# Performance work log

Hardware: AMD Instinct MI355X
Metric: run time of the kernel (lower is better)

## Reference

```python
import jax, jax.numpy as jnp
import numpy as np

EMBED = 1024
HEADS = 16
HEAD_DIM = EMBED // HEADS


def setup_inputs() -> dict:
    key = jax.random.key(0)
    ks = jax.random.split(key, 12)
    B, S, E = 2, 2048, EMBED
    scale = 1.0 / np.sqrt(E)
    inp = {
        "query": jax.random.normal(ks[0], (B, S, E), jnp.float32),
        "key": jax.random.normal(ks[1], (B, S, E), jnp.float32),
        "value": jax.random.normal(ks[2], (B, S, E), jnp.float32),
        "Wq": jax.random.normal(ks[3], (E, E), jnp.float32) * scale,
        "bq": jax.random.normal(ks[4], (E,), jnp.float32) * 0.01,
        "Wk": jax.random.normal(ks[5], (E, E), jnp.float32) * scale,
        "bk": jax.random.normal(ks[6], (E,), jnp.float32) * 0.01,
        "Wv": jax.random.normal(ks[7], (E, E), jnp.float32) * scale,
        "bv": jax.random.normal(ks[8], (E,), jnp.float32) * 0.01,
        "Wo": jax.random.normal(ks[9], (E, E), jnp.float32) * scale,
        "bo": jax.random.normal(ks[10], (E,), jnp.float32) * 0.01,
    }
    return inp


def reference(query, key, value, Wq, bq, Wk, bk, Wv, bv, Wo, bo):
    B, Sq, E = query.shape
    Sk = key.shape[1]
    H, D = HEADS, HEAD_DIM
    # QKV projections (torch Linear: x @ W.T + b)
    q = (query @ Wq.T + bq).reshape(B, Sq, H, D)
    k = (key @ Wk.T + bk).reshape(B, Sk, H, D)
    v = (value @ Wv.T + bv).reshape(B, Sk, H, D)
    # energy: [B, H, Sq, Sk]; note scale = 1/sqrt(embed_size), not head_dim
    energy = jnp.einsum("bqhd,bkhd->bhqk", q, k)
    scale = jnp.asarray(E, energy.dtype) ** 0.5
    attn = jax.nn.softmax(energy / scale, axis=-1)
    out = jnp.einsum("bhqk,bkhd->bqhd", attn, v).reshape(B, Sq, E)
    # fc_out (dropout is identity at eval)
    return out @ Wo.T + bo
```

## Files before the change

kernel.cpp:

```cpp
#include <hip/hip_runtime.h>
#include <hip/hip_bf16.h>

typedef __hip_bfloat16 bf16;
typedef short frag8 __attribute__((ext_vector_type(8)));
typedef _Float16 half4 __attribute__((ext_vector_type(4)));
typedef __fp16 fp16x2 __attribute__((ext_vector_type(2)));
typedef float f32x4 __attribute__((ext_vector_type(4)));

typedef __attribute__((address_space(3))) void lds_void;
typedef __attribute__((address_space(1))) const void gbl_void;

__device__ __forceinline__ void gld16(const void* g, void* l) {
  __builtin_amdgcn_global_load_lds((gbl_void*)g, (lds_void*)l, 16, 0, 0);
}

__device__ __forceinline__ unsigned short f2bf(float f) {
  union { float f; unsigned u; } x; x.f = f;
  unsigned r = x.u + 0x7FFFu + ((x.u >> 16) & 1u);
  return (unsigned short)(r >> 16);
}

#define QSCALE 0.0450842200278f
#define MFIX 4.0f

struct CvtArgs {
  const float4* src[7];
  ushort4* dst[7];
  int n4[7];
};
__global__ __launch_bounds__(256) void cvt_all(CvtArgs a) {
  const int t = blockIdx.y;
  const int i = blockIdx.x * 256 + threadIdx.x;
  if (i >= a.n4[t]) return;
  float4 v = a.src[t][i];
  ushort4 o;
  o.x = f2bf(v.x); o.y = f2bf(v.y); o.z = f2bf(v.z); o.w = f2bf(v.w);
  a.dst[t][i] = o;
}

template<int IH>
__device__ __forceinline__ void mfma16i(f32x4 (&acc)[8][4], const frag8 (&a4)[4], const frag8 (&b4)[4]) {
  __builtin_amdgcn_s_setprio(1);
  #pragma unroll
  for (int i = 0; i < 4; ++i) {
    #pragma unroll
    for (int j = 0; j < 4; ++j)
      acc[IH * 4 + i][j] = __builtin_amdgcn_mfma_f32_16x16x32_bf16(a4[i], b4[j], acc[IH * 4 + i][j], 0, 0, 0);
  }
  __builtin_amdgcn_s_setprio(0);
}

__global__ __launch_bounds__(512, 2)
void gemm_qkv256(const bf16* __restrict__ A0, const bf16* __restrict__ A1, const bf16* __restrict__ A2,
                 const bf16* __restrict__ W0, const bf16* __restrict__ W1, const bf16* __restrict__ W2,
                 const float* __restrict__ b0, const float* __restrict__ b1, const float* __restrict__ b2,
                 void* __restrict__ o0, void* __restrict__ o1, void* __restrict__ o2) {
  __shared__ __align__(16) bf16 As[2][16384];
  __shared__ __align__(16) bf16 Bs[2][16384];
  const int tid = threadIdx.x;
  const int wave = tid >> 6, lane = tid & 63, quad = lane >> 4, l16 = lane & 15;
  const int wm = wave >> 2, wn = wave & 3;
  const int bn = blockIdx.x, bm = blockIdx.y, z = blockIdx.z;

  const bf16* A = A0; const bf16* W = W0; const float* bias = b0; void* out = o0;
  if (z == 1) { A = A1; W = W1; bias = b1; out = o1; }
  else if (z == 2) { A = A2; W = W2; bias = b2; out = o2; }

  const bf16* Ab = A + (size_t)bm * 256 * 1024;
  const bf16* Wb = W + (size_t)bn * 256 * 1024;
  const int c0_ = tid & 3, r0_ = tid >> 2;
  const int gcp = ((c0_ ^ ((r0_ >> 1) & 3)) << 3);
  const int rc2 = (quad ^ ((l16 >> 1) & 3)) << 3;

  auto stage = [&](const bf16* src, int kt, int kh, bf16* dst) {
    #pragma unroll
    for (int is = 0; is < 2; ++is) {
      const int r = r0_ + is * 128;
      gld16(src + (size_t)r * 1024 + kt * 64 + kh * 32 + gcp,
            (void*)(dst + (is * 512 + tid) * 8));
    }
  };
  auto ldsA4 = [&](const bf16* ah, int ih, frag8 (&a4)[4]) {
    #pragma unroll
    for (int i = 0; i < 4; ++i)
      a4[i] = *(const frag8*)&ah[(wm * 128 + ih * 64 + i * 16 + l16) * 32 + rc2];
  };
  auto ldsB4 = [&](const bf16* bh, frag8 (&b4)[4]) {
    #pragma unroll
    for (int j = 0; j < 4; ++j)
      b4[j] = *(const frag8*)&bh[(wn * 64 + j * 16 + l16) * 32 + rc2];
  };

  f32x4 acc[8][4];
  #pragma unroll
  for (int i = 0; i < 8; ++i)
    #pragma unroll
    for (int j = 0; j < 4; ++j)
      acc[i][j] = (f32x4){0.f, 0.f, 0.f, 0.f};

  stage(Ab, 0, 0, &As[0][0]);
  stage(Wb, 0, 0, &Bs[0][0]);
  stage(Ab, 0, 1, &As[0][8192]);
  stage(Wb, 0, 1, &Bs[0][8192]);
  asm volatile("s_waitcnt vmcnt(0)" ::: "memory");
  __builtin_amdgcn_s_barrier();

  #pragma unroll 2
  for (int t = 0; t < 15; ++t) {
    const int buf = t & 1, nb = buf ^ 1;
    const bf16* a0 = &As[buf][0];    const bf16* a1 = &As[buf][8192];
    const bf16* b0 = &Bs[buf][0];    const bf16* b1 = &Bs[buf][8192];
    frag8 af[4], bf4[4];

    ldsA4(a0, 0, af); ldsB4(b0, bf4);
    stage(Ab, t + 1, 0, &As[nb][0]);
    __builtin_amdgcn_s_barrier();
    asm volatile("s_waitcnt lgkmcnt(0)" ::: "memory");
    mfma16i<0>(acc, af, bf4);
    __builtin_amdgcn_s_barrier();

    ldsA4(a0, 1, af);
    stage(Wb, t + 1, 0, &Bs[nb][0]);
    asm volatile("s_waitcnt vmcnt(4)" ::: "memory");
    __builtin_amdgcn_s_barrier();
    asm volatile("s_waitcnt lgkmcnt(0)" ::: "memory");
    mfma16i<1>(acc, af, bf4);
    __builtin_amdgcn_s_barrier();

    ldsA4(a1, 0, af); ldsB4(b1, bf4);
    stage(Ab, t + 1, 1, &As[nb][8192]);
    __builtin_amdgcn_s_barrier();
    asm volatile("s_waitcnt lgkmcnt(0)" ::: "memory");
    mfma16i<0>(acc, af, bf4);
    __builtin_amdgcn_s_barrier();

    ldsA4(a1, 1, af);
    stage(Wb, t + 1, 1, &Bs[nb][8192]);
    asm volatile("s_waitcnt vmcnt(4)" ::: "memory");
    __builtin_amdgcn_s_barrier();
    asm volatile("s_waitcnt lgkmcnt(0)" ::: "memory");
    mfma16i<1>(acc, af, bf4);
    __builtin_amdgcn_s_barrier();
  }

  {
    const bf16* a0 = &As[1][0];    const bf16* a1 = &As[1][8192];
    const bf16* b0 = &Bs[1][0];    const bf16* b1 = &Bs[1][8192];
    frag8 af[4], bf4[4];
    ldsA4(a0, 0, af); ldsB4(b0, bf4);
    asm volatile("s_waitcnt lgkmcnt(0)" ::: "memory");
    mfma16i<0>(acc, af, bf4);
    ldsA4(a0, 1, af);
    asm volatile("s_waitcnt lgkmcnt(0)" ::: "memory");
    mfma16i<1>(acc, af, bf4);
    asm volatile("s_waitcnt vmcnt(0)" ::: "memory");
    __builtin_amdgcn_s_barrier();
    ldsA4(a1, 0, af); ldsB4(b1, bf4);
    asm volatile("s_waitcnt lgkmcnt(0)" ::: "memory");
    mfma16i<0>(acc, af, bf4);
    ldsA4(a1, 1, af);
    asm volatile("s_waitcnt lgkmcnt(0)" ::: "memory");
    mfma16i<1>(acc, af, bf4);
  }

  #pragma unroll
  for (int j = 0; j < 4; ++j) {
    const int col = bn * 256 + wn * 64 + j * 16 + l16;
    const float bv = bias[col];
    #pragma unroll
    for (int i = 0; i < 8; ++i) {
      #pragma unroll
      for (int r = 0; r < 4; ++r) {
        const int row = bm * 256 + wm * 128 + i * 16 + quad * 4 + r;
        float v = acc[i][j][r] + bv;
        const int b = row >> 11, s = row & 2047;
        const int hh = col >> 6, d = col & 63;
        const size_t bh = (size_t)(b * 16 + hh);
        if (z == 0) {
          v *= QSCALE;
          ((bf16*)out)[(bh * 2048 + s) * 64 + d] = __float2bfloat16(v);
        } else if (z == 1) {
          const int rr = s & 127;
          const size_t addr = bh * 131072 + (size_t)(s >> 7) * 8192 + (size_t)rr * 64
                            + (size_t)(((d >> 3) ^ (rr & 7)) << 3) + (d & 7);
          ((bf16*)out)[addr] = __float2bfloat16(v);
        } else {
          const int kvl = s & 127;
          const size_t addr = bh * 131072 + (size_t)(s >> 7) * 8192 + (size_t)d * 128
                            + (size_t)((((kvl >> 2) ^ (d & 15)) << 2)) + (kvl & 3);
          ((_Float16*)out)[addr] = (_Float16)v;
        }
      }
    }
  }
}

template<int MODE>
__global__ __launch_bounds__(256)
void gemm_bt(const bf16* __restrict__ A0, const bf16* __restrict__ A1, const bf16* __restrict__ A2,
             const bf16* __restrict__ W0, const bf16* __restrict__ W1, const bf16* __restrict__ W2,
             const float* __restrict__ b0, const float* __restrict__ b1, const float* __restrict__ b2,
             void* __restrict__ o0, void* __restrict__ o1, void* __restrict__ o2) {
  constexpr int NK = 1024;
  constexpr int BN = (MODE == 1) ? 128 : 64;
  __shared__ __align__(16) bf16 As[2][128 * 32];
  __shared__ __align__(16) bf16 Bs[2][BN * 32];
  const int tid = threadIdx.x;
  const int wave = tid >> 6, lane = tid & 63, quad = lane >> 4, l16 = lane & 15;
  const int wm = wave >> 1, wn = wave & 1;
  const int bn = blockIdx.x, bm = blockIdx.y;

  const bf16* A = A0; const bf16* W = W0; const float* bias = b0; void* out = o0;

  const bf16* Ab = A + (size_t)bm * 128 * NK;
  const bf16* Wb = W + (size_t)bn * BN * NK;
  const int c0_ = tid & 3, r0_ = tid >> 2;
  const int rc = (quad ^ (l16 & 3)) << 3;

  auto stageA = [&](int k0, int buf) {
    #pragma unroll
    for (int is = 0; is < 2; ++is) {
      const int c = tid + is * 256;
      const int r = r0_ + is * 64;
      const int gc = (c0_ ^ (r & 3)) << 3;
      gld16(Ab + (size_t)r * NK + k0 + gc, (void*)(&As[buf][(size_t)c * 8]));
    }
  };
  auto stageW = [&](int k0, int buf) {
    const int r = r0_;
    const int gc = (c0_ ^ (r & 3)) << 3;
    gld16(Wb + (size_t)r * NK + k0 + gc, (void*)(&Bs[buf][(size_t)tid * 8]));
  };

  f32x4 acc[4][2];
  #pragma unroll
  for (int i = 0; i < 4; ++i)
    #pragma unroll
    for (int j = 0; j < 2; ++j)
      acc[i][j] = (f32x4){0.f, 0.f, 0.f, 0.f};

  stageA(0, 0); stageW(0, 0);
  #pragma unroll 2
  for (int kt = 0; kt < 32; ++kt) {
    __syncthreads();
    if (kt < 31) { stageA((kt + 1) * 32, (kt + 1) & 1); stageW((kt + 1) * 32, (kt + 1) & 1); }
    const bf16* as_ = As[kt & 1];
    const bf16* bs_ = Bs[kt & 1];
    frag8 af[4], bfr[2];
    #pragma unroll
    for (int i = 0; i < 4; ++i)
      af[i] = *(const frag8*)&as_[(wm * 64 + i * 16 + l16) * 32 + rc];
    #pragma unroll
    for (int j = 0; j < 2; ++j)
      bfr[j] = *(const frag8*)&bs_[(wn * 32 + j * 16 + l16) * 32 + rc];
    #pragma unroll
    for (int i = 0; i < 4; ++i)
      #pragma unroll
      for (int j = 0; j < 2; ++j)
        acc[i][j] = __builtin_amdgcn_mfma_f32_16x16x32_bf16(af[i], bfr[j], acc[i][j], 0, 0, 0);
  }

  #pragma unroll
  for (int j = 0; j < 2; ++j) {
    const int col = bn * 64 + wn * 32 + j * 16 + l16;
    const float bv = bias[col];
    #pragma unroll
    for (int i = 0; i < 4; ++i) {
      #pragma unroll
      for (int r = 0; r < 4; ++r) {
        const int row = bm * 128 + wm * 64 + i * 16 + quad * 4 + r;
        ((float*)out)[(size_t)row * 1024 + col] = acc[i][j][r] + bv;
      }
    }
  }
}

__global__ __launch_bounds__(512, 2)
void flash_attn(const bf16* __restrict__ Q, const bf16* __restrict__ K,
                const _Float16* __restrict__ Vt, bf16* __restrict__ ctx) {
  __shared__ __align__(16) char smem[65536];
  bf16* Ks = (bf16*)smem;
  _Float16* Vs = (_Float16*)(smem + 32768);
  const int tid = threadIdx.x;
  const int wave = tid >> 6, lane = tid & 63, quad = lane >> 4, l16 = lane & 15;
  const int qg = wave & 3, kvg = wave >> 2;
  const int bh = blockIdx.x, b = bh >> 4, h = bh & 15;
  const int q0 = blockIdx.y * 256 + qg * 64;
  const bf16* Qb = Q + (size_t)bh * 131072;
  const bf16* Kb = K + (size_t)bh * 131072;
  const _Float16* Vb = Vt + (size_t)bh * 131072;

  frag8 qf[4][2];
  #pragma unroll
  for (int qt = 0; qt < 4; ++qt)
    #pragma unroll
    for (int ks = 0; ks < 2; ++ks)
      qf[qt][ks] = *(const frag8*)(Qb + (size_t)(q0 + qt * 16 + l16) * 64 + ks * 32 + quad * 8);

  f32x4 rsv[4];
  f32x4 o[4][4];
  #pragma unroll
  for (int qt = 0; qt < 4; ++qt) {
    rsv[qt] = (f32x4){0.f, 0.f, 0.f, 0.f};
    #pragma unroll
    for (int dt = 0; dt < 4; ++dt)
      o[qt][dt] = (f32x4){0.f, 0.f, 0.f, 0.f};
  }

  const int xk = l16 & 7;
  const int vd = tid >> 3, vch = (tid & 7) << 3;

  auto stage = [&](int kt, int buf) {
    #pragma unroll
    for (int s = 0; s < 2; ++s) {
      const int g = s * 16 + kt;
      const size_t kgo = (size_t)(g >> 1) * 8192 + (size_t)(g & 1) * 4096;
      gld16(Kb + kgo + (size_t)tid * 8, (void*)(Ks + (s * 2 + buf) * 4096 + tid * 8));
      const size_t vgo = (size_t)(g >> 1) * 8192 + (size_t)(g & 1) * 64;
      gld16(Vb + vgo + (size_t)vd * 128 + vch, (void*)(Vs + (s * 2 + buf) * 4096 + tid * 8));
    }
  };

  stage(0, 0);
  #pragma unroll 2
  for (int kt = 0; kt < 16; ++kt) {
    __syncthreads();
    if (kt < 15) stage(kt + 1, (kt + 1) & 1);
    const bf16* ks_ = Ks + (kvg * 2 + (kt & 1)) * 4096;
    const _Float16* vs_ = Vs + (kvg * 2 + (kt & 1)) * 4096;

    f32x4 s[4][4];
    #pragma unroll
    for (int qt = 0; qt < 4; ++qt)
      #pragma unroll
      for (int jt = 0; jt < 4; ++jt)
        s[qt][jt] = (f32x4){-MFIX, -MFIX, -MFIX, -MFIX};
    #pragma unroll
    for (int ks = 0; ks < 2; ++ks) {
      frag8 kf[4];
      #pragma unroll
      for (int jt = 0; jt < 4; ++jt)
        kf[jt] = *(const frag8*)&ks_[(jt * 16 + l16) * 64 + (((ks * 4 + quad) ^ xk) << 3)];
      __builtin_amdgcn_s_setprio(1);
      #pragma unroll
      for (int qt = 0; qt < 4; ++qt)
        #pragma unroll
        for (int jt = 0; jt < 4; ++jt)
          s[qt][jt] = __builtin_amdgcn_mfma_f32_16x16x32_bf16(kf[jt], qf[qt][ks], s[qt][jt], 0, 0, 0);
      __builtin_amdgcn_s_setprio(0);
    }

    half4 pf[4][4];
    #pragma unroll
    for (int qt = 0; qt < 4; ++qt) {
      #pragma unroll
      for (int jt = 0; jt < 4; ++jt) {
        f32x4 p4;
        #pragma unroll
        for (int r = 0; r < 4; ++r)
          p4[r] = __builtin_amdgcn_exp2f(s[qt][jt][r]);
        rsv[qt] += p4;
        union { fp16x2 h2[2]; half4 h4; } u;
        u.h2[0] = __builtin_amdgcn_cvt_pkrtz(p4[0], p4[1]);
        u.h2[1] = __builtin_amdgcn_cvt_pkrtz(p4[2], p4[3]);
        pf[qt][jt] = u.h4;
      }
    }

    #pragma unroll
    for (int jt = 0; jt < 4; ++jt) {
      half4 vf[4];
      #pragma unroll
      for (int dt = 0; dt < 4; ++dt)
        vf[dt] = *(const half4*)&vs_[(dt * 16 + l16) * 64 + (((jt * 4 + quad) ^ l16) << 2)];
      __builtin_amdgcn_s_setprio(1);
      #pragma unroll
      for (int qt = 0; qt < 4; ++qt)
        #pragma unroll
        for (int dt = 0; dt < 4; ++dt)
          o[qt][dt] = __builtin_amdgcn_mfma_f32_16x16x16f16(vf[dt], pf[qt][jt], o[qt][dt], 0, 0, 0);
      __builtin_amdgcn_s_setprio(0);
    }
  }

  float4* mo = (float4*)smem;
  float*  ml = (float*)(smem + 32768);
  const int mbase = (qg * 64 + lane) * 8;
  #pragma unroll
  for (int r = 0; r < 2; ++r) {
    __syncthreads();
    if (kvg == 1) {
      #pragma unroll
      for (int qh = 0; qh < 2; ++qh) {
        const int qt = r * 2 + qh;
        #pragma unroll
        for (int dt = 0; dt < 4; ++dt) {
          const int i = qh * 4 + dt;
          mo[mbase + (i ^ (lane & 7))] = (float4){o[qt][dt][0], o[qt][dt][1], o[qt][dt][2], o[qt][dt][3]};
        }
        ml[(qg * 64 + lane) * 2 + qh] = rsv[qt][0] + rsv[qt][1] + rsv[qt][2] + rsv[qt][3];
      }
    }
    __syncthreads();
    if (kvg == 0) {
      #pragma unroll
      for (int qh = 0; qh < 2; ++qh) {
        const int qt = r * 2 + qh;
        float l = rsv[qt][0] + rsv[qt][1] + rsv[qt][2] + rsv[qt][3]
                + ml[(qg * 64 + lane) * 2 + qh];
        l += __shfl_xor(l, 16, 64);
        l += __shfl_xor(l, 32, 64);
        const float inv = __builtin_amdgcn_rcpf(l);
        const int q = q0 + qt * 16 + l16;
        #pragma unroll
        for (int dt = 0; dt < 4; ++dt) {
          const int i = qh * 4 + dt;
          const float4 po = mo[mbase + (i ^ (lane & 7))];
          ushort4 w;
          w.x = f2bf((o[qt][dt][0] + po.x) * inv);
          w.y = f2bf((o[qt][dt][1] + po.y) * inv);
          w.z = f2bf((o[qt][dt][2] + po.z) * inv);
          w.w = f2bf((o[qt][dt][3] + po.w) * inv);
          const int d = dt * 16 + quad * 4;
          *(uint2*)&ctx[((size_t)(b * 2048 + q)) * 1024 + h * 64 + d] = *(uint2*)&w;
        }
      }
    }
  }
}

extern "C" void kernel_launch(void* const* d_in, const int* in_sizes, int n_in,
                              void* d_out, int out_size, void* d_ws, size_t ws_size,
                              hipStream_t stream) {
  const float* q_in = (const float*)d_in[0];
  const float* k_in = (const float*)d_in[1];
  const float* v_in = (const float*)d_in[2];
  const float* Wq = (const float*)d_in[3];
  const float* bq = (const float*)d_in[4];
  const float* Wk = (const float*)d_in[5];
  const float* bk = (const float*)d_in[6];
  const float* Wv = (const float*)d_in[7];
  const float* bv = (const float*)d_in[8];
  const float* Wo = (const float*)d_in[9];
  const float* bo = (const float*)d_in[10];

  char* ws = (char*)d_ws;
  const size_t MB = 1024 * 1024;
  bf16* Xq  = (bf16*)(ws + 0 * MB);
  bf16* Xk  = (bf16*)(ws + 8 * MB);
  bf16* Xv  = (bf16*)(ws + 16 * MB);
  bf16* Wqb = (bf16*)(ws + 24 * MB);
  bf16* Wkb = (bf16*)(ws + 26 * MB);
  bf16* Wvb = (bf16*)(ws + 28 * MB);
  bf16* Wob = (bf16*)(ws + 30 * MB);
  bf16* Qw  = (bf16*)(ws + 32 * MB);
  bf16* Kw  = (bf16*)(ws + 40 * MB);
  _Float16* Vtw = (_Float16*)(ws + 48 * MB);
  bf16* Ctx = (bf16*)(ws + 56 * MB);

  {
    CvtArgs a;
    a.src[0] = (const float4*)q_in; a.dst[0] = (ushort4*)Xq;  a.n4[0] = 4194304 / 4;
    a.src[1] = (const float4*)k_in; a.dst[1] = (ushort4*)Xk;  a.n4[1] = 4194304 / 4;
    a.src[2] = (const float4*)v_in; a.dst[2] = (ushort4*)Xv;  a.n4[2] = 4194304 / 4;
    a.src[3] = (const float4*)Wq;   a.dst[3] = (ushort4*)Wqb; a.n4[3] = 1048576 / 4;
    a.src[4] = (const float4*)Wk;   a.dst[4] = (ushort4*)Wkb; a.n4[4] = 1048576 / 4;
    a.src[5] = (const float4*)Wv;   a.dst[5] = (ushort4*)Wvb; a.n4[5] = 1048576 / 4;
    a.src[6] = (const float4*)Wo;   a.dst[6] = (ushort4*)Wob; a.n4[6] = 1048576 / 4;
    cvt_all<<<dim3(4096, 7), 256, 0, stream>>>(a);
  }

  gemm_qkv256<<<dim3(4, 16, 3), 512, 0, stream>>>(Xq, Xk, Xv, Wqb, Wkb, Wvb,
                                                  bq, bk, bv, Qw, Kw, (bf16*)Vtw);
  flash_attn<<<dim3(32, 8), 512, 0, stream>>>(Qw, Kw, Vtw, Ctx);
  gemm_bt<0><<<dim3(16, 32), 256, 0, stream>>>(Ctx, nullptr, nullptr, Wob, nullptr, nullptr,
                                               bo, nullptr, nullptr, d_out, nullptr, nullptr);
}
```

Measured before the change: 226.7 us.

## Switch PV product to 16x16x32 f16 MFMA with regrouped K/V layouts

The P·V product now uses the 16x16x32 f16 MFMA on 8-wide fragments instead of the 16x16x16 variant, halving the MFMA instruction count. K rows are permuted within 64-key groups so each lane's 8 contiguous keys line up with the wider fragment. K and V are stored in contiguous 64-key tiles, which turns staging into plain linear copies. The risk is that the permutation must match the P register layout exactly, and the V swizzle changed, which may alter LDS bank conflicts.

```diff
diff --git a/kernel.cpp b/kernel.cpp
--- a/kernel.cpp
+++ b/kernel.cpp
@@ -4,6 +4,7 @@
 typedef __hip_bfloat16 bf16;
 typedef short frag8 __attribute__((ext_vector_type(8)));
 typedef _Float16 half4 __attribute__((ext_vector_type(4)));
+typedef _Float16 half8 __attribute__((ext_vector_type(8)));
 typedef __fp16 fp16x2 __attribute__((ext_vector_type(2)));
 typedef float f32x4 __attribute__((ext_vector_type(4)));
 
@@ -180,14 +181,16 @@
           v *= QSCALE;
           ((bf16*)out)[(bh * 2048 + s) * 64 + d] = __float2bfloat16(v);
         } else if (z == 1) {
-          const int rr = s & 127;
-          const size_t addr = bh * 131072 + (size_t)(s >> 7) * 8192 + (size_t)rr * 64
-                            + (size_t)(((d >> 3) ^ (rr & 7)) << 3) + (d & 7);
+          const int g = s >> 6, l32 = s & 31, G32 = (s >> 5) & 1;
+          const int q_ = (l32 >> 3) & 3, t_ = (l32 >> 2) & 1, i_ = l32 & 3;
+          const int r64 = G32 * 32 + t_ * 16 + q_ * 4 + i_;
+          const size_t addr = bh * 131072 + (size_t)g * 4096 + (size_t)r64 * 64
+                            + (size_t)(((d >> 3) ^ (r64 & 7)) << 3) + (d & 7);
           ((bf16*)out)[addr] = __float2bfloat16(v);
         } else {
-          const int kvl = s & 127;
-          const size_t addr = bh * 131072 + (size_t)(s >> 7) * 8192 + (size_t)d * 128
-                            + (size_t)((((kvl >> 2) ^ (d & 15)) << 2)) + (kvl & 3);
+          const int g = s >> 6, k = s & 63;
+          const size_t addr = bh * 131072 + (size_t)g * 4096 + (size_t)d * 64
+                            + (size_t)(((k >> 3) ^ (d & 7)) << 3) + (k & 7);
           ((_Float16*)out)[addr] = (_Float16)v;
         }
       }
@@ -308,16 +311,13 @@
   }
 
   const int xk = l16 & 7;
-  const int vd = tid >> 3, vch = (tid & 7) << 3;
 
   auto stage = [&](int kt, int buf) {
     #pragma unroll
     for (int s = 0; s < 2; ++s) {
       const int g = s * 16 + kt;
-      const size_t kgo = (size_t)(g >> 1) * 8192 + (size_t)(g & 1) * 4096;
-      gld16(Kb + kgo + (size_t)tid * 8, (void*)(Ks + (s * 2 + buf) * 4096 + tid * 8));
-      const size_t vgo = (size_t)(g >> 1) * 8192 + (size_t)(g & 1) * 64;
-      gld16(Vb + vgo + (size_t)vd * 128 + vch, (void*)(Vs + (s * 2 + buf) * 4096 + tid * 8));
+      gld16(Kb + (size_t)g * 4096 + (size_t)tid * 8, (void*)(Ks + (s * 2 + buf) * 4096 + tid * 8));
+      gld16(Vb + (size_t)g * 4096 + (size_t)tid * 8, (void*)(Vs + (s * 2 + buf) * 4096 + tid * 8));
     }
   };
 
@@ -350,7 +350,7 @@
       __builtin_amdgcn_s_setprio(0);
     }
 
-    half4 pf[4][4];
+    half8 pb[4][2];
     #pragma unroll
     for (int qt = 0; qt < 4; ++qt) {
       #pragma unroll
@@ -363,22 +363,26 @@
         union { fp16x2 h2[2]; half4 h4; } u;
         u.h2[0] = __builtin_amdgcn_cvt_pkrtz(p4[0], p4[1]);
         u.h2[1] = __builtin_amdgcn_cvt_pkrtz(p4[2], p4[3]);
-        pf[qt][jt] = u.h4;
+        const int jtp = jt >> 1, hi = (jt & 1) * 4;
+        pb[qt][jtp][hi + 0] = u.h4[0];
+        pb[qt][jtp][hi + 1] = u.h4[1];
+        pb[qt][jtp][hi + 2] = u.h4[2];
+        pb[qt][jtp][hi + 3] = u.h4[3];
       }
     }
 
     #pragma unroll
-    for (int jt = 0; jt < 4; ++jt) {
-      half4 vf[4];
+    for (int jtp = 0; jtp < 2; ++jtp) {
+      half8 vf[4];
       #pragma unroll
       for (int dt = 0; dt < 4; ++dt)
-        vf[dt] = *(const half4*)&vs_[(dt * 16 + l16) * 64 + (((jt * 4 + quad) ^ l16) << 2)];
+        vf[dt] = *(const half8*)&vs_[(dt * 16 + l16) * 64 + (((jtp * 4 + quad) ^ xk) << 3)];
       __builtin_amdgcn_s_setprio(1);
       #pragma unroll
       for (int qt = 0; qt < 4; ++qt)
         #pragma unroll
         for (int dt = 0; dt < 4; ++dt)
-          o[qt][dt] = __builtin_amdgcn_mfma_f32_16x16x16f16(vf[dt], pf[qt][jt], o[qt][dt], 0, 0, 0);
+          o[qt][dt] = __builtin_amdgcn_mfma_f32_16x16x32_f16(vf[dt], pb[qt][jtp], o[qt][dt], 0, 0, 0);
       __builtin_amdgcn_s_setprio(0);
     }
   }
```

New measurement: 227.3 us. About the same (+0.2%).
